# Kernel optimization log

Hardware: AMD Instinct MI355X
Metric: run time of the kernel (lower is better)

Reference implementation:

```python
import jax, jax.numpy as jnp
import numpy as np

D_MODEL = 1024
NHEAD = 16
D_K = D_MODEL // NHEAD


def setup_inputs() -> dict:
    key = jax.random.key(0)
    ks = jax.random.split(key, 8)
    B, S = 2, 2048
    scale = 1.0 / np.sqrt(D_MODEL)
    return {
        "Q": jax.random.normal(ks[0], (B, S, D_MODEL), dtype=jnp.float32),
        "K": jax.random.normal(ks[1], (B, S, D_MODEL), dtype=jnp.float32),
        "V": jax.random.normal(ks[2], (B, S, D_MODEL), dtype=jnp.float32),
        "WQ": jax.random.normal(ks[3], (D_MODEL, D_MODEL), dtype=jnp.float32) * scale,
        "WK": jax.random.normal(ks[4], (D_MODEL, D_MODEL), dtype=jnp.float32) * scale,
        "WV": jax.random.normal(ks[5], (D_MODEL, D_MODEL), dtype=jnp.float32) * scale,
        "Wfc": jax.random.normal(ks[6], (D_MODEL, D_MODEL), dtype=jnp.float32) * scale,
        "bfc": jax.random.normal(ks[7], (D_MODEL,), dtype=jnp.float32) * 0.01,
    }


def reference(Q, K, V, WQ, WK, WV, Wfc, bfc):
    B, Sq, _ = Q.shape
    Skv = K.shape[1]
    # Linear projections (torch Linear: x @ W^T), split into heads: [B, H, S, d_k]
    q = (Q @ WQ.T).reshape(B, Sq, NHEAD, D_K).transpose(0, 2, 1, 3)
    k = (K @ WK.T).reshape(B, Skv, NHEAD, D_K).transpose(0, 2, 1, 3)
    v = (V @ WV.T).reshape(B, Skv, NHEAD, D_K).transpose(0, 2, 1, 3)
    # Scaled dot-product scores: [B, H, Sq, Skv]
    scores = jnp.einsum("bhqd,bhkd->bhqk", q, k) / jnp.sqrt(jnp.float32(D_K))
    # Causal mask (strict upper triangle -> -inf)
    causal = jnp.tril(jnp.ones((Sq, Skv), dtype=bool))
    scores = jnp.where(causal, scores, -jnp.inf)
    attn = jax.nn.softmax(scores, axis=-1)
    y = jnp.einsum("bhqk,bhkd->bhqd", attn, v)
    y = y.transpose(0, 2, 1, 3).reshape(B, Sq, D_MODEL)
    return y @ Wfc.T + bfc
```

## Files before the change

### kernel.cpp

```cpp
#include <hip/hip_runtime.h>

typedef __attribute__((ext_vector_type(8))) short bf16x8;
typedef __attribute__((ext_vector_type(4))) float f32x4;
typedef __attribute__((ext_vector_type(16))) float f32x16;

__device__ __forceinline__ ushort f2bf(float f) {
    union { float f; unsigned u; } x; x.f = f;
    unsigned r = x.u + 0x7fffu + ((x.u >> 16) & 1u);
    return (ushort)(r >> 16);
}

__device__ __forceinline__ void async16(const void* g, void* l) {
    __builtin_amdgcn_global_load_lds(
        (const __attribute__((address_space(1))) void*)g,
        (__attribute__((address_space(3))) void*)l, 16, 0, 0);
}

__device__ __forceinline__ f32x4 mfma16(bf16x8 a, bf16x8 b, f32x4 c) {
    return __builtin_amdgcn_mfma_f32_16x16x32_bf16(a, b, c, 0, 0, 0);
}
__device__ __forceinline__ f32x16 mfma32(bf16x8 a, bf16x8 b, f32x16 c) {
    return __builtin_amdgcn_mfma_f32_32x32x16_bf16(a, b, c, 0, 0, 0);
}

__device__ __forceinline__ f32x4 zero4() { f32x4 z = {0.f, 0.f, 0.f, 0.f}; return z; }

__device__ __forceinline__ float xhalf_max(float v) {
    return fmaxf(v, __shfl_xor(v, 32));
}
__device__ __forceinline__ float xhalf_sum(float v) {
    return v + __shfl_xor(v, 32);
}

#define PIPE_BARRIER4(cond_more)                                         \
    do {                                                                 \
        if (cond_more) asm volatile("s_waitcnt vmcnt(4)" ::: "memory");  \
        else           asm volatile("s_waitcnt vmcnt(0)" ::: "memory");  \
        asm volatile("s_waitcnt lgkmcnt(0)" ::: "memory");               \
        __builtin_amdgcn_sched_barrier(0);                               \
        __builtin_amdgcn_s_barrier();                                    \
        __builtin_amdgcn_sched_barrier(0);                               \
    } while (0)

#define PIPE_BARRIER8(cond_more)                                         \
    do {                                                                 \
        if (cond_more) asm volatile("s_waitcnt vmcnt(8)" ::: "memory");  \
        else           asm volatile("s_waitcnt vmcnt(0)" ::: "memory");  \
        asm volatile("s_waitcnt lgkmcnt(0)" ::: "memory");               \
        __builtin_amdgcn_sched_barrier(0);                               \
        __builtin_amdgcn_s_barrier();                                    \
        __builtin_amdgcn_sched_barrier(0);                               \
    } while (0)

#define END_BARRIER()                                                    \
    do {                                                                 \
        asm volatile("s_waitcnt lgkmcnt(0)" ::: "memory");               \
        __builtin_amdgcn_sched_barrier(0);                               \
        __builtin_amdgcn_s_barrier();                                    \
        __builtin_amdgcn_sched_barrier(0);                               \
    } while (0)

__global__ void cvt7_kernel(
    const float* __restrict__ s0, const float* __restrict__ s1, const float* __restrict__ s2,
    const float* __restrict__ s3, const float* __restrict__ s4, const float* __restrict__ s5,
    const float* __restrict__ s6,
    ushort* __restrict__ d0, ushort* __restrict__ d1, ushort* __restrict__ d2,
    ushort* __restrict__ d3, ushort* __restrict__ d4, ushort* __restrict__ d5,
    ushort* __restrict__ d6)
{
    int y = blockIdx.y;
    const float* s; ushort* d; int n4;
    if      (y == 0) { s = s0; d = d0; n4 = 1048576; }
    else if (y == 1) { s = s1; d = d1; n4 = 1048576; }
    else if (y == 2) { s = s2; d = d2; n4 = 1048576; }
    else if (y == 3) { s = s3; d = d3; n4 = 262144; }
    else if (y == 4) { s = s4; d = d4; n4 = 262144; }
    else if (y == 5) { s = s5; d = d5; n4 = 262144; }
    else             { s = s6; d = d6; n4 = 262144; }
    int i = blockIdx.x * 256 + threadIdx.x;
    if (i >= n4) return;
    float4 v = ((const float4*)s)[i];
    ushort4 o;
    o.x = f2bf(v.x); o.y = f2bf(v.y); o.z = f2bf(v.z); o.w = f2bf(v.w);
    ((ushort4*)d)[i] = o;
}

template<bool SWAP>
__device__ __forceinline__ void gemm_core(
    const ushort* __restrict__ A, const ushort* __restrict__ W,
    char* smem, int bm, int bn, int tid, f32x4 acc[4][4])
{
    const int lane = tid & 63;
    const int wid  = tid >> 6;
    const int wr = wid >> 1, wc = wid & 1;
    const int l15 = lane & 15, g = lane >> 4;

    auto stage = [&](int kt) {
        char* As = smem + (kt & 1) * 32768;
        char* Bs = As + 16384;
        #pragma unroll
        for (int it = 0; it < 4; ++it) {
            int c = it * 256 + tid;
            int row = c >> 3, inner = c & 7;
            int srcoff = (inner ^ (row & 7)) * 16;
            async16((const char*)A + (size_t)(bm * 128 + row) * 2048 + kt * 128 + srcoff, As + c * 16);
            async16((const char*)W + (size_t)(bn * 128 + row) * 2048 + kt * 128 + srcoff, Bs + c * 16);
        }
    };

    stage(0);

    for (int kt = 0; kt < 16; ++kt) {
        const bool more = (kt < 15);
        if (more) stage(kt + 1);
        PIPE_BARRIER8(more);

        const char* As = smem + (kt & 1) * 32768;
        const char* Bs = As + 16384;
        bf16x8 af[4][2], bfr[4][2];
        #pragma unroll
        for (int mt = 0; mt < 4; ++mt)
            #pragma unroll
            for (int ks = 0; ks < 2; ++ks) {
                int row = wr * 64 + mt * 16 + l15;
                int byte = (row * 128 + ks * 64 + g * 16) ^ ((row & 7) << 4);
                af[mt][ks] = *(const bf16x8*)(As + byte);
            }
        #pragma unroll
        for (int nt = 0; nt < 4; ++nt)
            #pragma unroll
            for (int ks = 0; ks < 2; ++ks) {
                int row = wc * 64 + nt * 16 + l15;
                int byte = (row * 128 + ks * 64 + g * 16) ^ ((row & 7) << 4);
                bfr[nt][ks] = *(const bf16x8*)(Bs + byte);
            }
        __builtin_amdgcn_s_setprio(1);
        #pragma unroll
        for (int mt = 0; mt < 4; ++mt)
            #pragma unroll
            for (int nt = 0; nt < 4; ++nt)
                #pragma unroll
                for (int ks = 0; ks < 2; ++ks) {
                    if (SWAP) acc[mt][nt] = mfma16(bfr[nt][ks], af[mt][ks], acc[mt][nt]);
                    else      acc[mt][nt] = mfma16(af[mt][ks], bfr[nt][ks], acc[mt][nt]);
                }
        __builtin_amdgcn_s_setprio(0);
        END_BARRIER();
    }
}

__global__ __launch_bounds__(256, 2) void gemm_qkv(
    const ushort* __restrict__ Qb, const ushort* __restrict__ Kb, const ushort* __restrict__ Vb,
    const ushort* __restrict__ WQ, const ushort* __restrict__ WK, const ushort* __restrict__ WV,
    ushort* __restrict__ qhb, ushort* __restrict__ khb, ushort* __restrict__ vhT)
{
    __shared__ __align__(16) char smem[65536];
    const int tid = threadIdx.x;
    const int z  = blockIdx.x % 3;
    const int bm = blockIdx.x / 3;
    const int bn = blockIdx.y;
    const int lane = tid & 63;
    const int wid  = tid >> 6;
    const int wr = wid >> 1, wc = wid & 1;
    const int l15 = lane & 15, g = lane >> 4;

    const ushort* A  = (z == 0) ? Qb : (z == 1) ? Kb : Vb;
    const ushort* Wm = (z == 0) ? WQ : (z == 1) ? WK : WV;

    f32x4 acc[4][4];
    #pragma unroll
    for (int i = 0; i < 4; ++i)
        #pragma unroll
        for (int j = 0; j < 4; ++j) acc[i][j] = zero4();

    if (z == 2) {
        gemm_core<true>(A, Wm, smem, bm, bn, tid, acc);
        #pragma unroll
        for (int mt = 0; mt < 4; ++mt)
            #pragma unroll
            for (int nt = 0; nt < 4; ++nt)
                #pragma unroll
                for (int j = 0; j < 4; ++j) {
                    int n = bn * 128 + wc * 64 + nt * 16 + g * 4 + j;
                    int m = bm * 128 + wr * 64 + mt * 16 + l15;
                    int b = m >> 11, s = m & 2047, h = (n >> 6) & 15, d = n & 63;
                    vhT[(((size_t)(b * 16 + h)) * 64 + d) * 2048 + s] = f2bf(acc[mt][nt][j]);
                }
    } else {
        gemm_core<false>(A, Wm, smem, bm, bn, tid, acc);
        const float scale = (z == 0) ? 0.18033688011112042f : 1.0f;
        ushort* outb = (z == 0) ? qhb : khb;
        #pragma unroll
        for (int mt = 0; mt < 4; ++mt)
            #pragma unroll
            for (int nt = 0; nt < 4; ++nt)
                #pragma unroll
                for (int j = 0; j < 4; ++j) {
                    int m = bm * 128 + wr * 64 + mt * 16 + g * 4 + j;
                    int n = bn * 128 + wc * 64 + nt * 16 + l15;
                    int b = m >> 11, s = m & 2047, h = n >> 6, d = n & 63;
                    outb[(((size_t)(b * 16 + h)) * 2048 + s) * 64 + d] = f2bf(acc[mt][nt][j] * scale);
                }
    }
}

__global__ __launch_bounds__(256, 2) void gemm_fc(
    const ushort* __restrict__ A, const ushort* __restrict__ W,
    float* __restrict__ outf, const float* __restrict__ bias)
{
    __shared__ __align__(16) char smem[65536];
    const int tid = threadIdx.x;
    const int lane = tid & 63;
    const int wid  = tid >> 6;
    const int wr = wid >> 1, wc = wid & 1;
    const int l15 = lane & 15, g = lane >> 4;

    f32x4 acc[4][4];
    #pragma unroll
    for (int i = 0; i < 4; ++i)
        #pragma unroll
        for (int j = 0; j < 4; ++j) acc[i][j] = zero4();

    gemm_core<false>(A, W, smem, blockIdx.x, blockIdx.y, tid, acc);

    #pragma unroll
    for (int mt = 0; mt < 4; ++mt)
        #pragma unroll
        for (int nt = 0; nt < 4; ++nt)
            #pragma unroll
            for (int j = 0; j < 4; ++j) {
                int m = blockIdx.x * 128 + wr * 64 + mt * 16 + g * 4 + j;
                int n = blockIdx.y * 128 + wc * 64 + nt * 16 + l15;
                outf[(size_t)m * 1024 + n] = acc[mt][nt][j] + bias[n];
            }
}

__global__ __launch_bounds__(512, 2) void attn_kernel(
    const ushort* __restrict__ qh, const ushort* __restrict__ kh,
    const ushort* __restrict__ vhT, ushort* __restrict__ yb)
{
    __shared__ __align__(16) char smem[65536];
    const int tid = threadIdx.x;
    const int lane = tid & 63, wid = tid >> 6;
    const int l31 = lane & 31;
    const int hi  = lane >> 5;
    const int group = wid >> 2;
    const int wq    = wid & 3;
    const int subkv = group * 64;
    const int id = blockIdx.x;
    const int lo = id & 255;
    const int bh = (lo & 7) * 4 + ((lo >> 3) & 3);
    const int qt = (id < 256) ? (lo >> 5) : 15 - (lo >> 5);
    const size_t base = (size_t)bh * 2048 * 64;
    const int b_ = bh >> 4, h_ = bh & 15;
    const int qrw = qt * 128 + wq * 32;
    float* oml = (float*)smem;

    auto stageK = [&](int t, int b) {
        char* Ks = smem + b * 32768;
        #pragma unroll
        for (int it = 0; it < 2; ++it) {
            int c = it * 512 + tid;
            int row = c >> 3, inner = c & 7;
            async16((const char*)kh + (base + (size_t)(t * 128 + row) * 64) * 2 + ((inner ^ (row & 7)) * 16),
                    Ks + c * 16);
        }
    };
    auto stageV = [&](int t, int b) {
        char* Vs = smem + b * 32768 + 16384;
        #pragma unroll
        for (int it = 0; it < 2; ++it) {
            int c = it * 512 + tid;
            int row = c >> 4, inner = c & 15;
            async16((const char*)vhT + (base + (size_t)row * 2048 + (size_t)t * 128) * 2 + ((inner ^ (row & 15)) * 16),
                    Vs + c * 16);
        }
    };

    bf16x8 qf[4];
    #pragma unroll
    for (int ks = 0; ks < 4; ++ks)
        qf[ks] = *(const bf16x8*)((const char*)qh + (base + (size_t)(qrw + l31) * 64) * 2 + ks * 32 + hi * 16);

    f32x16 o[2];
    #pragma unroll
    for (int r = 0; r < 16; ++r) { o[0][r] = 0.f; o[1][r] = 0.f; }
    float m_run = -1e30f, l_run = 0.f;

    stageK(0, 0); stageV(0, 0);

    for (int t = 0; t <= qt; ++t) {
        const bool more = (t + 1 <= qt);
        if (more) { stageK(t + 1, (t + 1) & 1); stageV(t + 1, (t + 1) & 1); }
        PIPE_BARRIER4(more);

        const int kv0 = t * 128 + subkv;
        if (kv0 <= qrw + 31) {
            const char* Ks = smem + (t & 1) * 32768;
            const char* Vs = Ks + 16384;

            f32x16 st[2];
            #pragma unroll
            for (int r = 0; r < 16; ++r) { st[0][r] = 0.f; st[1][r] = 0.f; }
            #pragma unroll
            for (int tt = 0; tt < 2; ++tt) {
                bf16x8 kf[4];
                #pragma unroll
                for (int ks = 0; ks < 4; ++ks) {
                    int krow = subkv + tt * 32 + l31;
                    int byte = (krow * 128 + ks * 32 + hi * 16) ^ ((krow & 7) << 4);
                    kf[ks] = *(const bf16x8*)(Ks + byte);
                }
                __builtin_amdgcn_s_setprio(1);
                #pragma unroll
                for (int ks = 0; ks < 4; ++ks)
                    st[tt] = mfma32(kf[ks], qf[ks], st[tt]);
                __builtin_amdgcn_s_setprio(0);
            }

            bf16x8 vf[4][2];
            #pragma unroll
            for (int ks = 0; ks < 4; ++ks)
                #pragma unroll
                for (int dt = 0; dt < 2; ++dt) {
                    int vrow = dt * 32 + l31;
                    int colB = subkv * 2 + ks * 32 + hi * 16;
                    int byte = vrow * 256 + (colB ^ ((vrow & 15) << 4));
                    vf[ks][dt] = *(const bf16x8*)(Vs + byte);
                }

            if (kv0 + 63 > qrw) {
                #pragma unroll
                for (int tt = 0; tt < 2; ++tt)
                    #pragma unroll
                    for (int r = 0; r < 16; ++r) {
                        int kv = kv0 + tt * 32 + (r & 3) + 8 * (r >> 2) + 4 * hi;
                        if (kv > qrw + l31) st[tt][r] = -1e30f;
                    }
            }

            float mx;
            {
                float t0[8];
                #pragma unroll
                for (int r = 0; r < 8; ++r)
                    t0[r] = fmaxf(fmaxf(st[0][r], st[0][r + 8]),
                                  fmaxf(st[1][r], st[1][r + 8]));
                float t1[4];
                #pragma unroll
                for (int r = 0; r < 4; ++r) t1[r] = fmaxf(t0[r], t0[r + 4]);
                mx = fmaxf(fmaxf(t1[0], t1[2]), fmaxf(t1[1], t1[3]));
            }
            mx = xhalf_max(mx);

            if (!__all(mx - m_run <= 8.0f)) {
                float mn = fmaxf(m_run, mx);
                float corr = __builtin_amdgcn_exp2f(m_run - mn);
                l_run *= corr;
                m_run = mn;
                #pragma unroll
                for (int r = 0; r < 16; ++r) {
                    int qsrc = (r & 3) + 8 * (r >> 2) + 4 * hi;
                    float c2 = __shfl(corr, qsrc);
                    o[0][r] *= c2; o[1][r] *= c2;
                }
            }

            #pragma unroll
            for (int tt = 0; tt < 2; ++tt)
                #pragma unroll
                for (int r = 0; r < 16; ++r)
                    st[tt][r] = __builtin_amdgcn_exp2f(st[tt][r] - m_run);
            float sum;
            {
                float s0[8];
                #pragma unroll
                for (int r = 0; r < 8; ++r)
                    s0[r] = (st[0][r] + st[0][r + 8]) + (st[1][r] + st[1][r + 8]);
                float s1[4];
                #pragma unroll
                for (int r = 0; r < 4; ++r) s1[r] = s0[r] + s0[r + 4];
                sum = (s1[0] + s1[2]) + (s1[1] + s1[3]);
            }
            sum = xhalf_sum(sum);
            l_run += sum;

            unsigned Wd[2][8], Xw[2][8];
            #pragma unroll
            for (int tt = 0; tt < 2; ++tt)
                #pragma unroll
                for (int k = 0; k < 8; ++k) {
                    unsigned w;
                    asm("v_cvt_pk_bf16_f32 %0, %1, %2" : "=v"(w) : "v"(st[tt][2 * k]), "v"(st[tt][2 * k + 1]));
                    Wd[tt][k] = w;
                }
            #pragma unroll
            for (int tt = 0; tt < 2; ++tt)
                #pragma unroll
                for (int k = 0; k < 8; ++k)
                    Xw[tt][k] = __shfl_xor((int)Wd[tt][k], 32);

            #pragma unroll
            for (int ks = 0; ks < 4; ++ks) {
                const int t2 = ks >> 1, bse = (ks & 1) * 4;
                unsigned w0 = hi ? Xw[t2][bse + 2] : Wd[t2][bse + 0];
                unsigned w1 = hi ? Xw[t2][bse + 3] : Wd[t2][bse + 1];
                unsigned w2 = hi ? Wd[t2][bse + 2] : Xw[t2][bse + 0];
                unsigned w3 = hi ? Wd[t2][bse + 3] : Xw[t2][bse + 1];
                unsigned pw4[4] = {w0, w1, w2, w3};
                bf16x8 pf = *(const bf16x8*)pw4;
                __builtin_amdgcn_s_setprio(1);
                #pragma unroll
                for (int dt = 0; dt < 2; ++dt)
                    o[dt] = mfma32(pf, vf[ks][dt], o[dt]);
                __builtin_amdgcn_s_setprio(0);
            }
        }
        END_BARRIER();
    }

    if (group == 1) {
        float* pp = oml + (size_t)(wq * 64 + lane) * 36;
        #pragma unroll
        for (int r = 0; r < 16; ++r) { pp[r] = o[0][r]; pp[16 + r] = o[1][r]; }
        pp[32] = m_run; pp[33] = l_run;
    }
    __syncthreads();
    if (group == 0) {
        const float* pp = oml + (size_t)(wq * 64 + lane) * 36;
        float m1 = pp[32], l1 = pp[33];
        float mn = fmaxf(m_run, m1);
        float a0 = __builtin_amdgcn_exp2f(m_run - mn);
        float a1 = __builtin_amdgcn_exp2f(m1 - mn);
        float lt = l_run * a0 + l1 * a1;
        float invl = 1.0f / lt;
        #pragma unroll
        for (int r = 0; r < 16; ++r) {
            int qsrc = (r & 3) + 8 * (r >> 2) + 4 * hi;
            float f0 = __shfl(a0, qsrc);
            float f1 = __shfl(a1, qsrc);
            float iv = __shfl(invl, qsrc);
            float v0 = (o[0][r] * f0 + pp[r] * f1) * iv;
            float v1 = (o[1][r] * f0 + pp[16 + r] * f1) * iv;
            int q = qrw + qsrc;
            size_t rowoff = ((size_t)(b_ * 2048 + q)) * 1024 + h_ * 64;
            yb[rowoff + l31]      = f2bf(v0);
            yb[rowoff + 32 + l31] = f2bf(v1);
        }
    }
}

extern "C" void kernel_launch(void* const* d_in, const int* in_sizes, int n_in,
                              void* d_out, int out_size, void* d_ws, size_t ws_size,
                              hipStream_t stream)
{
    const size_t MD = 4096ull * 1024;
    const size_t WD = 1024ull * 1024;
    ushort* ws  = (ushort*)d_ws;
    ushort* Qb  = ws;
    ushort* Kb  = Qb + MD;
    ushort* Vb  = Kb + MD;
    ushort* qhb = Vb + MD;
    ushort* khb = qhb + MD;
    ushort* vhT = khb + MD;
    ushort* WQb = vhT + MD;
    ushort* WKb = WQb + WD;
    ushort* WVb = WKb + WD;
    ushort* Wfb = WVb + WD;
    ushort* yb  = Qb;

    cvt7_kernel<<<dim3(4096, 7), 256, 0, stream>>>(
        (const float*)d_in[0], (const float*)d_in[1], (const float*)d_in[2],
        (const float*)d_in[3], (const float*)d_in[4], (const float*)d_in[5],
        (const float*)d_in[6],
        Qb, Kb, Vb, WQb, WKb, WVb, Wfb);

    gemm_qkv<<<dim3(96, 8), 256, 0, stream>>>(Qb, Kb, Vb, WQb, WKb, WVb, qhb, khb, vhT);
    attn_kernel<<<512, 512, 0, stream>>>(qhb, khb, vhT, yb);
    gemm_fc<<<dim3(32, 8), 256, 0, stream>>>(yb, Wfb, (float*)d_out, (const float*)d_in[7]);
}
```

Measured before the change: 106.2 us.

## Fuse fp32-to-bf16 activation conversion into QKV projection GEMM loads

The QKV GEMM now reads the fp32 Q/K/V activations directly into registers, converts them to bf16 with packed conversions, and writes them to swizzled LDS. This lets the separate conversion kernel handle only the four weight matrices. The aim is to drop a full write and re-read of 24 MB of bf16 activations plus part of a launch. The cost is that A-tile loads are no longer async-to-LDS: they hold registers across the MFMA phase and add VALU conversion and LDS store work per K step, with a new vmcnt(12) wait count.

Result: no change. 104.7 us (-1.4%).

```diff
diff --git a/kernel.cpp b/kernel.cpp
--- a/kernel.cpp
+++ b/kernel.cpp
@@ -25,6 +25,12 @@
 
 __device__ __forceinline__ f32x4 zero4() { f32x4 z = {0.f, 0.f, 0.f, 0.f}; return z; }
 
+__device__ __forceinline__ unsigned cvtpk(float lo, float hi) {
+    unsigned w;
+    asm("v_cvt_pk_bf16_f32 %0, %1, %2" : "=v"(w) : "v"(lo), "v"(hi));
+    return w;
+}
+
 __device__ __forceinline__ float xhalf_max(float v) {
     return fmaxf(v, __shfl_xor(v, 32));
 }
@@ -32,24 +38,14 @@
     return v + __shfl_xor(v, 32);
 }
 
-#define PIPE_BARRIER4(cond_more)                                         \
-    do {                                                                 \
-        if (cond_more) asm volatile("s_waitcnt vmcnt(4)" ::: "memory");  \
-        else           asm volatile("s_waitcnt vmcnt(0)" ::: "memory");  \
-        asm volatile("s_waitcnt lgkmcnt(0)" ::: "memory");               \
-        __builtin_amdgcn_sched_barrier(0);                               \
-        __builtin_amdgcn_s_barrier();                                    \
-        __builtin_amdgcn_sched_barrier(0);                               \
-    } while (0)
-
-#define PIPE_BARRIER8(cond_more)                                         \
-    do {                                                                 \
-        if (cond_more) asm volatile("s_waitcnt vmcnt(8)" ::: "memory");  \
-        else           asm volatile("s_waitcnt vmcnt(0)" ::: "memory");  \
-        asm volatile("s_waitcnt lgkmcnt(0)" ::: "memory");               \
-        __builtin_amdgcn_sched_barrier(0);                               \
-        __builtin_amdgcn_s_barrier();                                    \
-        __builtin_amdgcn_sched_barrier(0);                               \
+#define PIPE_BARRIER_N(N, cond_more)                                        \
+    do {                                                                    \
+        if (cond_more) asm volatile("s_waitcnt vmcnt(" #N ")" ::: "memory");\
+        else           asm volatile("s_waitcnt vmcnt(0)" ::: "memory");     \
+        asm volatile("s_waitcnt lgkmcnt(0)" ::: "memory");                  \
+        __builtin_amdgcn_sched_barrier(0);                                  \
+        __builtin_amdgcn_s_barrier();                                       \
+        __builtin_amdgcn_sched_barrier(0);                                  \
     } while (0)
 
 #define END_BARRIER()                                                    \
@@ -60,29 +56,125 @@
         __builtin_amdgcn_sched_barrier(0);                               \
     } while (0)
 
-__global__ void cvt7_kernel(
-    const float* __restrict__ s0, const float* __restrict__ s1, const float* __restrict__ s2,
-    const float* __restrict__ s3, const float* __restrict__ s4, const float* __restrict__ s5,
-    const float* __restrict__ s6,
-    ushort* __restrict__ d0, ushort* __restrict__ d1, ushort* __restrict__ d2,
-    ushort* __restrict__ d3, ushort* __restrict__ d4, ushort* __restrict__ d5,
-    ushort* __restrict__ d6)
+__global__ void cvt4_kernel(
+    const float* __restrict__ s0, const float* __restrict__ s1,
+    const float* __restrict__ s2, const float* __restrict__ s3,
+    ushort* __restrict__ d0, ushort* __restrict__ d1,
+    ushort* __restrict__ d2, ushort* __restrict__ d3)
 {
     int y = blockIdx.y;
-    const float* s; ushort* d; int n4;
-    if      (y == 0) { s = s0; d = d0; n4 = 1048576; }
-    else if (y == 1) { s = s1; d = d1; n4 = 1048576; }
-    else if (y == 2) { s = s2; d = d2; n4 = 1048576; }
-    else if (y == 3) { s = s3; d = d3; n4 = 262144; }
-    else if (y == 4) { s = s4; d = d4; n4 = 262144; }
-    else if (y == 5) { s = s5; d = d5; n4 = 262144; }
-    else             { s = s6; d = d6; n4 = 262144; }
+    const float* s; ushort* d;
+    if      (y == 0) { s = s0; d = d0; }
+    else if (y == 1) { s = s1; d = d1; }
+    else if (y == 2) { s = s2; d = d2; }
+    else             { s = s3; d = d3; }
     int i = blockIdx.x * 256 + threadIdx.x;
-    if (i >= n4) return;
     float4 v = ((const float4*)s)[i];
     ushort4 o;
     o.x = f2bf(v.x); o.y = f2bf(v.y); o.z = f2bf(v.z); o.w = f2bf(v.w);
     ((ushort4*)d)[i] = o;
+}
+
+template<bool SWAP>
+__device__ __forceinline__ void gemm_core_f32a(
+    const float* __restrict__ A32, const ushort* __restrict__ W,
+    char* smem, int bm, int bn, int tid, f32x4 acc[4][4])
+{
+    const int lane = tid & 63;
+    const int wid  = tid >> 6;
+    const int wr = wid >> 1, wc = wid & 1;
+    const int l15 = lane & 15, g = lane >> 4;
+
+    int rowc[4], eoffc[4];
+    #pragma unroll
+    for (int it = 0; it < 4; ++it) {
+        int c = it * 256 + tid;
+        rowc[it]  = c >> 3;
+        eoffc[it] = ((c & 7) ^ (rowc[it] & 7)) * 8;
+    }
+
+    auto loadA = [&](int kt, float4 r[4][2]) {
+        #pragma unroll
+        for (int it = 0; it < 4; ++it) {
+            const float* p = A32 + (size_t)(bm * 128 + rowc[it]) * 1024 + kt * 64 + eoffc[it];
+            r[it][0] = *(const float4*)p;
+            r[it][1] = *(const float4*)(p + 4);
+        }
+    };
+    auto stageB = [&](int kt) {
+        char* Bs = smem + (kt & 1) * 32768 + 16384;
+        #pragma unroll
+        for (int it = 0; it < 4; ++it) {
+            int c = it * 256 + tid;
+            int row = c >> 3, inner = c & 7;
+            int srcoff = (inner ^ (row & 7)) * 16;
+            async16((const char*)W + (size_t)(bn * 128 + row) * 2048 + kt * 128 + srcoff,
+                    smem + (kt & 1) * 32768 + 16384 + c * 16);
+            (void)Bs;
+        }
+    };
+    auto writeA = [&](int kt, const float4 r[4][2]) {
+        char* As = smem + (kt & 1) * 32768;
+        #pragma unroll
+        for (int it = 0; it < 4; ++it) {
+            int c = it * 256 + tid;
+            unsigned w[4];
+            w[0] = cvtpk(r[it][0].x, r[it][0].y);
+            w[1] = cvtpk(r[it][0].z, r[it][0].w);
+            w[2] = cvtpk(r[it][1].x, r[it][1].y);
+            w[3] = cvtpk(r[it][1].z, r[it][1].w);
+            *(bf16x8*)(As + c * 16) = *(const bf16x8*)w;
+        }
+    };
+
+    {
+        float4 r0[4][2];
+        loadA(0, r0);
+        stageB(0);
+        writeA(0, r0);
+    }
+
+    for (int kt = 0; kt < 16; ++kt) {
+        const bool more = (kt < 15);
+        float4 rn[4][2];
+        if (more) { loadA(kt + 1, rn); stageB(kt + 1); }
+        PIPE_BARRIER_N(12, more);
+
+        const char* As = smem + (kt & 1) * 32768;
+        const char* Bs = As + 16384;
+        bf16x8 af[4][2], bfr[4][2];
+        #pragma unroll
+        for (int mt = 0; mt < 4; ++mt)
+            #pragma unroll
+            for (int ks = 0; ks < 2; ++ks) {
+                int row = wr * 64 + mt * 16 + l15;
+                int byte = (row * 128 + ks * 64 + g * 16) ^ ((row & 7) << 4);
+                af[mt][ks] = *(const bf16x8*)(As + byte);
+            }
+        #pragma unroll
+        for (int nt = 0; nt < 4; ++nt)
+            #pragma unroll
+            for (int ks = 0; ks < 2; ++ks) {
+                int row = wc * 64 + nt * 16 + l15;
+                int byte = (row * 128 + ks * 64 + g * 16) ^ ((row & 7) << 4);
+                bfr[nt][ks] = *(const bf16x8*)(Bs + byte);
+            }
+        __builtin_amdgcn_s_setprio(1);
+        #pragma unroll
+        for (int mt = 0; mt < 4; ++mt)
+            #pragma unroll
+            for (int nt = 0; nt < 4; ++nt)
+                #pragma unroll
+                for (int ks = 0; ks < 2; ++ks) {
+                    if (SWAP) acc[mt][nt] = mfma16(bfr[nt][ks], af[mt][ks], acc[mt][nt]);
+                    else      acc[mt][nt] = mfma16(af[mt][ks], bfr[nt][ks], acc[mt][nt]);
+                }
+        __builtin_amdgcn_s_setprio(0);
+
+        if (more) writeA(kt + 1, rn);
+
+        END_BARRIER();
+    }
 }
 
 template<bool SWAP>
@@ -113,7 +205,7 @@
     for (int kt = 0; kt < 16; ++kt) {
         const bool more = (kt < 15);
         if (more) stage(kt + 1);
-        PIPE_BARRIER8(more);
+        PIPE_BARRIER_N(8, more);
 
         const char* As = smem + (kt & 1) * 32768;
         const char* Bs = As + 16384;
@@ -150,7 +242,7 @@
 }
 
 __global__ __launch_bounds__(256, 2) void gemm_qkv(
-    const ushort* __restrict__ Qb, const ushort* __restrict__ Kb, const ushort* __restrict__ Vb,
+    const float* __restrict__ Q32, const float* __restrict__ K32, const float* __restrict__ V32,
     const ushort* __restrict__ WQ, const ushort* __restrict__ WK, const ushort* __restrict__ WV,
     ushort* __restrict__ qhb, ushort* __restrict__ khb, ushort* __restrict__ vhT)
 {
@@ -164,7 +256,7 @@
     const int wr = wid >> 1, wc = wid & 1;
     const int l15 = lane & 15, g = lane >> 4;
 
-    const ushort* A  = (z == 0) ? Qb : (z == 1) ? Kb : Vb;
+    const float*  A  = (z == 0) ? Q32 : (z == 1) ? K32 : V32;
     const ushort* Wm = (z == 0) ? WQ : (z == 1) ? WK : WV;
 
     f32x4 acc[4][4];
@@ -174,7 +266,7 @@
         for (int j = 0; j < 4; ++j) acc[i][j] = zero4();
 
     if (z == 2) {
-        gemm_core<true>(A, Wm, smem, bm, bn, tid, acc);
+        gemm_core_f32a<true>(A, Wm, smem, bm, bn, tid, acc);
         #pragma unroll
         for (int mt = 0; mt < 4; ++mt)
             #pragma unroll
@@ -187,7 +279,7 @@
                     vhT[(((size_t)(b * 16 + h)) * 64 + d) * 2048 + s] = f2bf(acc[mt][nt][j]);
                 }
     } else {
-        gemm_core<false>(A, Wm, smem, bm, bn, tid, acc);
+        gemm_core_f32a<false>(A, Wm, smem, bm, bn, tid, acc);
         const float scale = (z == 0) ? 0.18033688011112042f : 1.0f;
         ushort* outb = (z == 0) ? qhb : khb;
         #pragma unroll
@@ -292,7 +384,7 @@
     for (int t = 0; t <= qt; ++t) {
         const bool more = (t + 1 <= qt);
         if (more) { stageK(t + 1, (t + 1) & 1); stageV(t + 1, (t + 1) & 1); }
-        PIPE_BARRIER4(more);
+        PIPE_BARRIER_N(4, more);
 
         const int kv0 = t * 128 + subkv;
         if (kv0 <= qrw + 31) {
@@ -389,11 +481,8 @@
             #pragma unroll
             for (int tt = 0; tt < 2; ++tt)
                 #pragma unroll
-                for (int k = 0; k < 8; ++k) {
-                    unsigned w;
-                    asm("v_cvt_pk_bf16_f32 %0, %1, %2" : "=v"(w) : "v"(st[tt][2 * k]), "v"(st[tt][2 * k + 1]));
-                    Wd[tt][k] = w;
-                }
+                for (int k = 0; k < 8; ++k)
+                    Wd[tt][k] = cvtpk(st[tt][2 * k], st[tt][2 * k + 1]);
             #pragma unroll
             for (int tt = 0; tt < 2; ++tt)
                 #pragma unroll
@@ -469,13 +558,14 @@
     ushort* Wfb = WVb + WD;
     ushort* yb  = Qb;
 
-    cvt7_kernel<<<dim3(4096, 7), 256, 0, stream>>>(
-        (const float*)d_in[0], (const float*)d_in[1], (const float*)d_in[2],
+    cvt4_kernel<<<dim3(1024, 4), 256, 0, stream>>>(
         (const float*)d_in[3], (const float*)d_in[4], (const float*)d_in[5],
         (const float*)d_in[6],
-        Qb, Kb, Vb, WQb, WKb, WVb, Wfb);
-
-    gemm_qkv<<<dim3(96, 8), 256, 0, stream>>>(Qb, Kb, Vb, WQb, WKb, WVb, qhb, khb, vhT);
+        WQb, WKb, WVb, Wfb);
+
+    gemm_qkv<<<dim3(96, 8), 256, 0, stream>>>(
+        (const float*)d_in[0], (const float*)d_in[1], (const float*)d_in[2],
+        WQb, WKb, WVb, qhb, khb, vhT);
     attn_kernel<<<512, 512, 0, stream>>>(qhb, khb, vhT, yb);
     gemm_fc<<<dim3(32, 8), 256, 0, stream>>>(yb, Wfb, (float*)d_out, (const float*)d_in[7]);
 }
```
